# Performance work log

Hardware: AMD Instinct MI355X
Metric: run time of the kernel (lower is better)

Reference implementation:

```python
import jax, jax.numpy as jnp
import numpy as np
from jax import lax

B, S, H, T = 64, 512, 1024, 48


def setup_inputs() -> dict:
    key = jax.random.key(0)
    ks = jax.random.split(key, 8)
    x = jax.random.normal(ks[0], (B, S, H), dtype=jnp.float32)
    # left-aligned variable-length attention mask (lengths in [S//2, S])
    lengths = jax.random.randint(ks[1], (B,), S // 2, S + 1)
    attention_mask = (jnp.arange(S)[None, :] < lengths[:, None]).astype(jnp.int32)
    labels = jax.random.randint(ks[2], (B, S), 0, T).astype(jnp.int64)
    # decoder Linear(H, T)
    W = jax.random.normal(ks[3], (H, T), dtype=jnp.float32) / np.sqrt(H)
    b = jnp.zeros((T,), dtype=jnp.float32)
    # CRF parameters (allennlp-style: transitions + start/end transitions)
    transitions = jax.random.normal(ks[4], (T, T), dtype=jnp.float32) * 0.1
    start_trans = jax.random.normal(ks[5], (T,), dtype=jnp.float32) * 0.1
    end_trans = jax.random.normal(ks[6], (T,), dtype=jnp.float32) * 0.1
    return {"x": x, "attention_mask": attention_mask, "labels": labels,
            "W": W, "b": b, "transitions": transitions,
            "start_trans": start_trans, "end_trans": end_trans}


def _log_partition(logits, mask, trans, start, end):
    # logits [B,S,T], mask [B,S] int. Returns logZ [B].
    alpha0 = start[None, :] + logits[:, 0]                     # [B,T]
    emits = jnp.moveaxis(logits[:, 1:], 1, 0)                  # [S-1,B,T]
    ms = mask[:, 1:].T                                         # [S-1,B]

    def step(alpha, inp):
        emit, m = inp
        inner = alpha[:, :, None] + trans[None, :, :] + emit[:, None, :]  # [B,T,T]
        new = jax.nn.logsumexp(inner, axis=1)
        alpha = jnp.where(m[:, None] > 0, new, alpha)
        return alpha, None

    alpha, _ = lax.scan(step, alpha0, (emits, ms))
    return jax.nn.logsumexp(alpha + end[None, :], axis=1)      # [B]


def _gold_score(logits, labels, mask, trans, start, end):
    maskf = mask.astype(logits.dtype)
    emit = jnp.take_along_axis(logits, labels[..., None], axis=2)[..., 0]  # [B,S]
    emit_score = jnp.sum(emit * maskf, axis=1)
    tr = trans[labels[:, :-1], labels[:, 1:]]                   # [B,S-1]
    trans_score = jnp.sum(tr * maskf[:, 1:], axis=1)
    last_idx = jnp.sum(mask, axis=1) - 1                        # [B]
    last_tags = jnp.take_along_axis(labels, last_idx[:, None], axis=1)[:, 0]
    return start[labels[:, 0]] + emit_score + trans_score + end[last_tags]


def _viterbi(logits, mask, trans, start, end):
    Bn, Sn, Tn = logits.shape
    v0 = start[None, :] + logits[:, 0]
    emits = jnp.moveaxis(logits[:, 1:], 1, 0)                  # [S-1,B,T]
    ms = mask[:, 1:].T
    ident = jnp.broadcast_to(jnp.arange(Tn, dtype=jnp.int32)[None, :], (Bn, Tn))

    def step(v, inp):
        emit, m = inp
        scores = v[:, :, None] + trans[None, :, :]              # [B,T_prev,T_cur]
        bp = jnp.argmax(scores, axis=1).astype(jnp.int32)       # [B,T]
        best = jnp.max(scores, axis=1) + emit
        v_new = jnp.where(m[:, None] > 0, best, v)
        bp = jnp.where(m[:, None] > 0, bp, ident)               # identity at padded steps
        return v_new, bp

    v, bps = lax.scan(step, v0, (emits, ms))                    # bps [S-1,B,T]
    last = jnp.argmax(v + end[None, :], axis=1).astype(jnp.int32)  # [B]

    def back(tag, bp):
        prev = jnp.take_along_axis(bp, tag[:, None], axis=1)[:, 0]
        return prev, tag

    first_tag, rest = lax.scan(back, last, bps, reverse=True)   # rest [S-1,B]
    tags = jnp.concatenate([first_tag[:, None], rest.T], axis=1)  # [B,S]
    return (tags * mask).astype(jnp.int64)                      # pad with zeros


def reference(x, attention_mask, labels, W, b, transitions, start_trans, end_trans):
    features = jnp.einsum('bsh,ht->bst', x, W) + b              # decoder Linear
    pred_labels = _viterbi(features, attention_mask, transitions, start_trans, end_trans)
    logZ = _log_partition(features, attention_mask, transitions, start_trans, end_trans)
    gold = _gold_score(features, labels, attention_mask, transitions, start_trans, end_trans)
    loss = -jnp.sum(gold - logZ)                                # -log-likelihood, summed over batch
    return features, pred_labels, loss
```

## Files before the change

### kernel.cpp

```cpp
#include <hip/hip_runtime.h>
#include <hip/hip_bf16.h>
#include <math.h>

#define Bn 64
#define Sn 512
#define Hn 1024
#define Tn 48

#define LOG2E 1.4426950408889634f
#define LN2f  0.6931471805599453f

#define PRED_OFF (Bn*Sn*Tn)
#define LOSS_OFF (PRED_OFF + Bn*Sn)

#define RL(x,i) __int_as_float(__builtin_amdgcn_readlane(__float_as_int(x),(i)))

#if __has_builtin(__builtin_amdgcn_exp2f)
#define EXP2(x) __builtin_amdgcn_exp2f(x)
#else
#define EXP2(x) exp2f(x)
#endif
#if __has_builtin(__builtin_amdgcn_logf)
#define LOG2(x) __builtin_amdgcn_logf(x)
#else
#define LOG2(x) log2f(x)
#endif

__device__ __forceinline__ unsigned umin2(unsigned a, unsigned b) { return a < b ? a : b; }

#define VWS_BYTE_OFF 512
#define BPW_BYTE_OFF (512 + (size_t)Bn*Sn*Tn*4)

#define DOT4(ACC,A,B) { ACC = fmaf((A).x,(B).x,ACC); ACC = fmaf((A).y,(B).y,ACC); ACC = fmaf((A).z,(B).z,ACC); ACC = fmaf((A).w,(B).w,ACC); }

__global__ __launch_bounds__(256) void gemm_feat(
    const float* __restrict__ x, const float* __restrict__ W,
    const float* __restrict__ bias, float* __restrict__ feat)
{
  __shared__ __align__(16) float xs[64][68];
  __shared__ __align__(16) float wsT[Tn][68];
  const int tid = threadIdx.x;
  const int srow = tid >> 2;
  const int sqc  = tid & 3;
  const int ty = tid >> 3;
  const int tx = tid & 7;
  const size_t row0 = (size_t)blockIdx.x * 64;

  float4 xreg[4];
  float  wreg[12];
  #pragma unroll
  for (int p = 0; p < 4; ++p)
    xreg[p] = *reinterpret_cast<const float4*>(&x[(row0 + srow)*Hn + (sqc + p*4)*4]);
  #pragma unroll
  for (int i = 0; i < 12; ++i) {
    const int id = tid + i*256; const int kk = id/Tn; const int t = id - kk*Tn;
    wreg[i] = W[(size_t)kk*Tn + t];
  }

  float acc[2][6];
  #pragma unroll
  for (int r = 0; r < 2; ++r)
    #pragma unroll
    for (int c = 0; c < 6; ++c) acc[r][c] = 0.f;

  for (int k0 = 0; k0 < Hn; k0 += 64) {
    #pragma unroll
    for (int p = 0; p < 4; ++p)
      *reinterpret_cast<float4*>(&xs[srow][(sqc + p*4)*4]) = xreg[p];
    #pragma unroll
    for (int i = 0; i < 12; ++i) {
      const int id = tid + i*256; const int kk = id/Tn; const int t = id - kk*Tn;
      wsT[t][kk] = wreg[i];
    }
    __syncthreads();
    if (k0 + 64 < Hn) {
      #pragma unroll
      for (int p = 0; p < 4; ++p)
        xreg[p] = *reinterpret_cast<const float4*>(&x[(row0 + srow)*Hn + (k0+64) + (sqc + p*4)*4]);
      #pragma unroll
      for (int i = 0; i < 12; ++i) {
        const int id = tid + i*256; const int kk = id/Tn; const int t = id - kk*Tn;
        wreg[i] = W[(size_t)(k0 + 64 + kk)*Tn + t];
      }
    }
    #pragma unroll 4
    for (int kk = 0; kk < 64; kk += 4) {
      const float4 a0 = *reinterpret_cast<const float4*>(&xs[ty*2+0][kk]);
      const float4 a1 = *reinterpret_cast<const float4*>(&xs[ty*2+1][kk]);
      const float4 w0 = *reinterpret_cast<const float4*>(&wsT[tx*6+0][kk]);
      const float4 w1 = *reinterpret_cast<const float4*>(&wsT[tx*6+1][kk]);
      const float4 w2 = *reinterpret_cast<const float4*>(&wsT[tx*6+2][kk]);
      const float4 w3 = *reinterpret_cast<const float4*>(&wsT[tx*6+3][kk]);
      const float4 w4 = *reinterpret_cast<const float4*>(&wsT[tx*6+4][kk]);
      const float4 w5 = *reinterpret_cast<const float4*>(&wsT[tx*6+5][kk]);
      DOT4(acc[0][0],a0,w0) DOT4(acc[0][1],a0,w1) DOT4(acc[0][2],a0,w2)
      DOT4(acc[0][3],a0,w3) DOT4(acc[0][4],a0,w4) DOT4(acc[0][5],a0,w5)
      DOT4(acc[1][0],a1,w0) DOT4(acc[1][1],a1,w1) DOT4(acc[1][2],a1,w2)
      DOT4(acc[1][3],a1,w3) DOT4(acc[1][4],a1,w4) DOT4(acc[1][5],a1,w5)
    }
    __syncthreads();
  }
  #pragma unroll
  for (int c = 0; c < 6; ++c) {
    const int col = tx*6 + c;
    const float bv = bias[col];
    #pragma unroll
    for (int r = 0; r < 2; ++r)
      feat[(row0 + ty*2 + r)*Tn + col] = acc[r][c] + bv;
  }
}

__device__ __forceinline__ int seq_len(const int* __restrict__ mask, int b, int lane) {
  int lc = 0;
  #pragma unroll
  for (int it = 0; it < Sn/64; ++it) lc += (mask[(size_t)b*Sn + it*64 + lane] != 0);
  #pragma unroll
  for (int off = 32; off; off >>= 1) lc += __shfl_xor(lc, off);
  return lc;
}

#define ETS 52

__global__ __launch_bounds__(64, 1) void crf_scan(
    const float* __restrict__ feat,
    const int* __restrict__ mask,
    const int* __restrict__ labels,
    const float* __restrict__ trans,
    const float* __restrict__ startv,
    const float* __restrict__ endv,
    float* __restrict__ vws,
    float* __restrict__ wsLogZ,
    float* __restrict__ wsGold)
{
  __shared__ __align__(16) float LB[64 + 48*ETS];

  const int role = blockIdx.x >> 6;
  const int b    = blockIdx.x & 63;
  const int lane = threadIdx.x;
  const float* fb = feat + (size_t)b * Sn * Tn;
  const int len = seq_len(mask, b, lane);
  const int j = (lane < Tn) ? lane : (Tn - 1);

  const float4* sv4 = reinterpret_cast<const float4*>(&LB[0]);
  const float4* et4 = reinterpret_cast<const float4*>(&LB[64 + j*ETS]);

  if (role == 0) {
    for (int idx = lane; idx < Tn*Tn; idx += 64) {
      const int ii = idx / Tn, jj = idx - (idx/Tn)*Tn;
      LB[64 + jj*ETS + ii] = EXP2(trans[idx] * LOG2E);
    }
    __syncthreads();
    float emq0,emq1,emq2,emq3,emq4,emq5,emq6,emq7;
    #define LDEM(u) { int s = 1 + u; s = s < len ? s : len - 1; emq##u = fb[(size_t)s*Tn + j]; }
    LDEM(0) LDEM(1) LDEM(2) LDEM(3) LDEM(4) LDEM(5) LDEM(6) LDEM(7)
    #undef LDEM
    const float a0 = (startv[j] + fb[j]) * LOG2E;
    float Zref = RL(a0, 0);
    float beta = a0 - Zref;
    LB[lane] = EXP2(beta);
    #define PSTEP(u) { const int tt = t + u; if (tt < len) { \
      const float em2 = emq##u * LOG2E; \
      int tf = tt + 8; tf = tf < len ? tf : len - 1; \
      emq##u = fb[(size_t)tf * Tn + j]; \
      float s0=0.f,s1=0.f,s2=0.f,s3=0.f; \
      _Pragma("unroll") \
      for (int r = 0; r < 12; ++r) { \
        const float4 pv = sv4[r]; \
        const float4 ev = et4[r]; \
        s0 = fmaf(pv.x, ev.x, s0); \
        s1 = fmaf(pv.y, ev.y, s1); \
        s2 = fmaf(pv.z, ev.z, s2); \
        s3 = fmaf(pv.w, ev.w, s3); \
      } \
      const float dj = LOG2((s0+s1)+(s2+s3)) + em2; \
      const float d0 = RL(dj,0); \
      Zref += d0; beta = dj - d0; \
      LB[lane] = EXP2(beta); } }
    for (int t = 1; t < len; t += 8) {
      PSTEP(0) PSTEP(1) PSTEP(2) PSTEP(3) PSTEP(4) PSTEP(5) PSTEP(6) PSTEP(7)
    }
    #undef PSTEP
    float fv = (lane < Tn) ? beta + endv[lane] * LOG2E : -INFINITY;
    float m = fv;
    #pragma unroll
    for (int off = 32; off; off >>= 1) m = fmaxf(m, __shfl_xor(m, off));
    float e = (lane < Tn) ? EXP2(fv - m) : 0.f;
    #pragma unroll
    for (int off = 32; off; off >>= 1) e += __shfl_xor(e, off);
    if (lane == 0) wsLogZ[b] = (Zref + m + LOG2(e)) * LN2f;

  } else if (role == 1) {
    for (int idx = lane; idx < Tn*Tn; idx += 64) {
      const int ii = idx / Tn, jj = idx - (idx/Tn)*Tn;
      LB[64 + jj*ETS + ii] = trans[idx];
    }
    __syncthreads();
    float emq0,emq1,emq2,emq3,emq4,emq5,emq6,emq7;
    #define LDEM(u) { int s = 1 + u; s = s < len ? s : len - 1; emq##u = fb[(size_t)s*Tn + j]; }
    LDEM(0) LDEM(1) LDEM(2) LDEM(3) LDEM(4) LDEM(5) LDEM(6) LDEM(7)
    #undef LDEM
    float v = startv[j] + fb[j];
    LB[lane] = v;
    if (lane < Tn) vws[(size_t)b*Sn*Tn + lane] = v;
    #define VSTEP(u) { const int tt = t + u; if (tt < len) { \
      const float em_cur = emq##u; \
      int tf = tt + 8; tf = tf < len ? tf : len - 1; \
      emq##u = fb[(size_t)tf * Tn + j]; \
      float g0 = -INFINITY, g1 = -INFINITY, g2 = -INFINITY, g3 = -INFINITY; \
      _Pragma("unroll") \
      for (int r = 0; r < 12; ++r) { \
        const float4 pv = sv4[r]; \
        const float4 tv = et4[r]; \
        g0 = fmaxf(g0, pv.x + tv.x); \
        g1 = fmaxf(g1, pv.y + tv.y); \
        g2 = fmaxf(g2, pv.z + tv.z); \
        g3 = fmaxf(g3, pv.w + tv.w); \
      } \
      const float best = fmaxf(fmaxf(g0,g1), fmaxf(g2,g3)); \
      v = best + em_cur; \
      LB[lane] = v; \
      if (lane < Tn) vws[((size_t)b*Sn + tt)*Tn + lane] = v; } }
    for (int t = 1; t < len; t += 8) {
      VSTEP(0) VSTEP(1) VSTEP(2) VSTEP(3) VSTEP(4) VSTEP(5) VSTEP(6) VSTEP(7)
    }
    #undef VSTEP

  } else {
    float g = 0.f;
    #pragma unroll
    for (int it = 0; it < Sn/64; ++it) {
      const int sg = it*64 + lane;
      if (sg < len) {
        const int la = labels[(size_t)b*Sn + sg];
        float e = fb[(size_t)sg*Tn + la];
        if (sg > 0) e += trans[labels[(size_t)b*Sn + sg - 1]*Tn + la];
        g += e;
      }
    }
    #pragma unroll
    for (int off = 32; off; off >>= 1) g += __shfl_xor(g, off);
    if (lane == 0) {
      g += startv[labels[(size_t)b*Sn]] + endv[labels[(size_t)b*Sn + len - 1]];
      wsGold[b] = g;
    }
  }
}

__global__ __launch_bounds__(256) void bp_kernel(
    const float* __restrict__ vws,
    const int* __restrict__ mask,
    const float* __restrict__ trans,
    unsigned char* __restrict__ bpw)
{
  const int b    = blockIdx.x >> 3;
  const int oct  = blockIdx.x & 7;
  const int wv   = threadIdx.x >> 6;
  const int lane = threadIdx.x & 63;
  const int len = seq_len(mask, b, lane);
  const int j = (lane < Tn) ? lane : (Tn - 1);

  float4 T0,T1,T2,T3,T4,T5,T6,T7,T8,T9,T10,T11;
  #define LDT(k) T##k.x = trans[(4*k+0)*Tn + j]; \
                 T##k.y = trans[(4*k+1)*Tn + j]; \
                 T##k.z = trans[(4*k+2)*Tn + j]; \
                 T##k.w = trans[(4*k+3)*Tn + j];
  LDT(0) LDT(1) LDT(2) LDT(3) LDT(4) LDT(5) LDT(6) LDT(7) LDT(8) LDT(9) LDT(10) LDT(11)
  #undef LDT

  const int t0 = oct*64 + wv*16;
  for (int i = 0; i < 16; ++i) {
    const int t = t0 + i;
    int te = t; te = te < 1 ? 1 : te; te = te < len ? te : len - 1;
    const float4* vp = reinterpret_cast<const float4*>(vws + ((size_t)b*Sn + te - 1)*Tn);
    #define LDA(k) const float4 A##k = vp[k];
    LDA(0) LDA(1) LDA(2) LDA(3) LDA(4) LDA(5) LDA(6) LDA(7) LDA(8) LDA(9) LDA(10) LDA(11)
    #undef LDA
    #define GMAX(k) const float gq##k = fmaxf( \
      fmaxf(A##k.x+T##k.x, A##k.y+T##k.y), fmaxf(A##k.z+T##k.z, A##k.w+T##k.w));
    GMAX(0) GMAX(1) GMAX(2) GMAX(3) GMAX(4) GMAX(5)
    GMAX(6) GMAX(7) GMAX(8) GMAX(9) GMAX(10) GMAX(11)
    #undef GMAX
    const float h0 = fmaxf(fmaxf(gq0,gq1),fmaxf(gq2,gq3));
    const float h1 = fmaxf(fmaxf(gq4,gq5),fmaxf(gq6,gq7));
    const float h2 = fmaxf(fmaxf(gq8,gq9),fmaxf(gq10,gq11));
    const float best = fmaxf(fmaxf(h0,h1),h2);
    #define KEYG(k) umin2( \
      umin2(__float_as_uint((A##k.x+T##k.x)-best)|(unsigned)(4*k+0), \
            __float_as_uint((A##k.y+T##k.y)-best)|(unsigned)(4*k+1)), \
      umin2(__float_as_uint((A##k.z+T##k.z)-best)|(unsigned)(4*k+2), \
            __float_as_uint((A##k.w+T##k.w)-best)|(unsigned)(4*k+3)))
    const unsigned kA = umin2(umin2(KEYG(0), KEYG(1)), umin2(KEYG(2), KEYG(3)));
    const unsigned kB = umin2(umin2(KEYG(4), KEYG(5)), umin2(KEYG(6), KEYG(7)));
    const unsigned kC = umin2(umin2(KEYG(8), KEYG(9)), umin2(KEYG(10), KEYG(11)));
    #undef KEYG
    const unsigned bidx = umin2(umin2(kA, kB), kC);
    if (t >= 1 && t < len && lane < Tn)
      bpw[((size_t)b*Sn + t)*Tn + lane] = (unsigned char)bidx;
  }
}

__device__ __forceinline__ unsigned idw(int a) {
  return (unsigned)a | ((unsigned)(a+1)<<8) | ((unsigned)(a+2)<<16) | ((unsigned)(a+3)<<24);
}

__global__ __launch_bounds__(64, 1) void backtrace_kernel(
    const float* __restrict__ vws,
    const unsigned char* __restrict__ bpw,
    const int* __restrict__ mask,
    const float* __restrict__ endv,
    float* __restrict__ pred_out)
{
  __shared__ unsigned char bpL[Sn * Tn];
  __shared__ unsigned char pathL[384 * 64];
  __shared__ int EA[8];

  const int b    = blockIdx.x;
  const int lane = threadIdx.x;
  const int len = seq_len(mask, b, lane);

  {
    const uint4* gb = reinterpret_cast<const uint4*>(bpw + (size_t)b*Sn*Tn);
    uint4* bl = reinterpret_cast<uint4*>(bpL);
    for (int i4 = lane; i4 < Sn*Tn/16; i4 += 64) {
      const int byte0 = i4*16;
      const int t = byte0 / Tn;
      const int j0 = byte0 - t*Tn;
      uint4 val;
      if (t >= 1 && t < len) val = gb[i4];
      else { val.x = idw(j0); val.y = idw(j0+4); val.z = idw(j0+8); val.w = idw(j0+12); }
      bl[i4] = val;
    }
  }

  float fv = (lane < Tn) ? vws[((size_t)b*Sn + len - 1)*Tn + lane] + endv[lane] : -INFINITY;
  int fi = (lane < Tn) ? lane : 64;
  #pragma unroll
  for (int off = 32; off; off >>= 1) {
    const float ov = __shfl_xor(fv, off);
    const int   oi = __shfl_xor(fi, off);
    if (ov > fv || (ov == fv && oi < fi)) { fv = ov; fi = oi; }
  }
  __syncthreads();

  #define JOB(r) \
    const int id##r  = lane + 64*(r); \
    const int seg##r = id##r & 7;     \
    int cur##r = id##r >> 3;          \
    const int bpb##r = seg##r * 64 * Tn; \
    const int pb##r  = id##r << 6;    \
    pathL[pb##r + 63] = (unsigned char)cur##r;
  JOB(0) JOB(1) JOB(2) JOB(3) JOB(4) JOB(5)
  for (int d = 62; d >= 0; --d) {
    const int o = (d + 1) * Tn;
    cur0 = bpL[bpb0 + o + cur0]; pathL[pb0 + d] = (unsigned char)cur0;
    cur1 = bpL[bpb1 + o + cur1]; pathL[pb1 + d] = (unsigned char)cur1;
    cur2 = bpL[bpb2 + o + cur2]; pathL[pb2 + d] = (unsigned char)cur2;
    cur3 = bpL[bpb3 + o + cur3]; pathL[pb3 + d] = (unsigned char)cur3;
    cur4 = bpL[bpb4 + o + cur4]; pathL[pb4 + d] = (unsigned char)cur4;
    cur5 = bpL[bpb5 + o + cur5]; pathL[pb5 + d] = (unsigned char)cur5;
  }
  #undef JOB
  __syncthreads();
  if (lane == 0) {
    int Ecur = fi;
    EA[7] = Ecur;
    for (int s = 7; s >= 1; --s) {
      const int bottom = pathL[((Ecur << 3) + s) * 64];
      Ecur = bpL[(s * 64) * Tn + bottom];
      EA[s-1] = Ecur;
    }
  }
  __syncthreads();
  #pragma unroll
  for (int r8 = 0; r8 < 8; ++r8) {
    const int t = r8*64 + lane;
    const int pv = pathL[((EA[r8] << 3) + r8) * 64 + lane];
    pred_out[(size_t)b*Sn + t] = (t < len) ? (float)pv : 0.f;
  }
}

__global__ void loss_reduce(const float* __restrict__ wsLogZ,
                            const float* __restrict__ wsGold,
                            float* __restrict__ out)
{
  const int lane = threadIdx.x;
  float v = wsLogZ[lane] - wsGold[lane];
  #pragma unroll
  for (int off = 32; off; off >>= 1) v += __shfl_xor(v, off);
  if (lane == 0) out[0] = v;
}

extern "C" void kernel_launch(void* const* d_in, const int* in_sizes, int n_in,
                              void* d_out, int out_size, void* d_ws, size_t ws_size,
                              hipStream_t stream) {
  const float* x      = (const float*)d_in[0];
  const int*   mask   = (const int*)  d_in[1];
  const int*   labels = (const int*)  d_in[2];
  const float* W      = (const float*)d_in[3];
  const float* bias   = (const float*)d_in[4];
  const float* trans  = (const float*)d_in[5];
  const float* startv = (const float*)d_in[6];
  const float* endv   = (const float*)d_in[7];

  float* out  = (float*)d_out;
  float* feat = out;
  float* pred = out + PRED_OFF;
  float* loss = out + LOSS_OFF;
  float* wsLogZ = (float*)d_ws;
  float* wsGold = wsLogZ + 64;
  float* vws = (float*)((char*)d_ws + VWS_BYTE_OFF);
  unsigned char* bpw = (unsigned char*)d_ws + BPW_BYTE_OFF;

  gemm_feat<<<(Bn*Sn)/64, 256, 0, stream>>>(x, W, bias, feat);
  crf_scan<<<192, 64, 0, stream>>>(feat, mask, labels, trans, startv, endv, vws, wsLogZ, wsGold);
  bp_kernel<<<512, 256, 0, stream>>>(vws, mask, trans, bpw);
  backtrace_kernel<<<64, 64, 0, stream>>>(vws, bpw, mask, endv, pred);
  loss_reduce<<<1, 64, 0, stream>>>(wsLogZ, wsGold, loss);
}
```

Before: 343.1 us.

## Pack 16 CRF scan jobs per 1024-thread block sharing transition tables

Repacks the CRF scan from 192 single-wave blocks into 12 blocks of 16 waves, each wave handling one (role, batch) job. The transition tables, both exp and raw, are built once per block in shared memory instead of once per wave, and each wave gets its own 64-float state slot. The inner 12-step loops are manually unrolled through macros. This concentrates the serial scans on only 12 CUs with 16 waves each, which may contend for LDS bandwidth and issue slots compared with spreading them across many CUs.

New measurement: 399.7 us. 16.5% more time.

```diff
diff --git a/kernel.cpp b/kernel.cpp
--- a/kernel.cpp
+++ b/kernel.cpp
@@ -121,7 +121,7 @@
 
 #define ETS 52
 
-__global__ __launch_bounds__(64, 1) void crf_scan(
+__global__ __launch_bounds__(1024, 1) void crf_scan(
     const float* __restrict__ feat,
     const int* __restrict__ mask,
     const int* __restrict__ labels,
@@ -132,24 +132,34 @@
     float* __restrict__ wsLogZ,
     float* __restrict__ wsGold)
 {
-  __shared__ __align__(16) float LB[64 + 48*ETS];
-
-  const int role = blockIdx.x >> 6;
-  const int b    = blockIdx.x & 63;
-  const int lane = threadIdx.x;
+  __shared__ __align__(16) float ST[16*64];
+  __shared__ __align__(16) float TE[48*ETS];
+  __shared__ __align__(16) float TT[48*ETS];
+
+  const int tid  = threadIdx.x;
+  const int w    = tid >> 6;
+  const int lane = tid & 63;
+  const int job  = w * 12 + blockIdx.x;
+  const int role = job >> 6;
+  const int b    = job & 63;
+
+  for (int idx = tid; idx < Tn*Tn; idx += 1024) {
+    const int ii = idx / Tn, jj = idx - (idx/Tn)*Tn;
+    const float tv = trans[idx];
+    TE[jj*ETS + ii] = EXP2(tv * LOG2E);
+    TT[jj*ETS + ii] = tv;
+  }
+  __syncthreads();
+
   const float* fb = feat + (size_t)b * Sn * Tn;
   const int len = seq_len(mask, b, lane);
   const int j = (lane < Tn) ? lane : (Tn - 1);
 
-  const float4* sv4 = reinterpret_cast<const float4*>(&LB[0]);
-  const float4* et4 = reinterpret_cast<const float4*>(&LB[64 + j*ETS]);
+  float* sw = &ST[w * 64];
+  const float4* sv4 = reinterpret_cast<const float4*>(sw);
 
   if (role == 0) {
-    for (int idx = lane; idx < Tn*Tn; idx += 64) {
-      const int ii = idx / Tn, jj = idx - (idx/Tn)*Tn;
-      LB[64 + jj*ETS + ii] = EXP2(trans[idx] * LOG2E);
-    }
-    __syncthreads();
+    const float4* et4 = reinterpret_cast<const float4*>(&TE[j*ETS]);
     float emq0,emq1,emq2,emq3,emq4,emq5,emq6,emq7;
     #define LDEM(u) { int s = 1 + u; s = s < len ? s : len - 1; emq##u = fb[(size_t)s*Tn + j]; }
     LDEM(0) LDEM(1) LDEM(2) LDEM(3) LDEM(4) LDEM(5) LDEM(6) LDEM(7)
@@ -157,29 +167,28 @@
     const float a0 = (startv[j] + fb[j]) * LOG2E;
     float Zref = RL(a0, 0);
     float beta = a0 - Zref;
-    LB[lane] = EXP2(beta);
+    sw[lane] = EXP2(beta);
+    #define FMAG(k) { const float4 pv = sv4[k]; const float4 ev = et4[k]; \
+      s0 = fmaf(pv.x, ev.x, s0); \
+      s1 = fmaf(pv.y, ev.y, s1); \
+      s2 = fmaf(pv.z, ev.z, s2); \
+      s3 = fmaf(pv.w, ev.w, s3); }
     #define PSTEP(u) { const int tt = t + u; if (tt < len) { \
       const float em2 = emq##u * LOG2E; \
       int tf = tt + 8; tf = tf < len ? tf : len - 1; \
       emq##u = fb[(size_t)tf * Tn + j]; \
       float s0=0.f,s1=0.f,s2=0.f,s3=0.f; \
-      _Pragma("unroll") \
-      for (int r = 0; r < 12; ++r) { \
-        const float4 pv = sv4[r]; \
-        const float4 ev = et4[r]; \
-        s0 = fmaf(pv.x, ev.x, s0); \
-        s1 = fmaf(pv.y, ev.y, s1); \
-        s2 = fmaf(pv.z, ev.z, s2); \
-        s3 = fmaf(pv.w, ev.w, s3); \
-      } \
+      FMAG(0) FMAG(1) FMAG(2) FMAG(3) FMAG(4) FMAG(5) \
+      FMAG(6) FMAG(7) FMAG(8) FMAG(9) FMAG(10) FMAG(11) \
       const float dj = LOG2((s0+s1)+(s2+s3)) + em2; \
       const float d0 = RL(dj,0); \
       Zref += d0; beta = dj - d0; \
-      LB[lane] = EXP2(beta); } }
+      sw[lane] = EXP2(beta); } }
     for (int t = 1; t < len; t += 8) {
       PSTEP(0) PSTEP(1) PSTEP(2) PSTEP(3) PSTEP(4) PSTEP(5) PSTEP(6) PSTEP(7)
     }
     #undef PSTEP
+    #undef FMAG
     float fv = (lane < Tn) ? beta + endv[lane] * LOG2E : -INFINITY;
     float m = fv;
     #pragma unroll
@@ -190,40 +199,35 @@
     if (lane == 0) wsLogZ[b] = (Zref + m + LOG2(e)) * LN2f;
 
   } else if (role == 1) {
-    for (int idx = lane; idx < Tn*Tn; idx += 64) {
-      const int ii = idx / Tn, jj = idx - (idx/Tn)*Tn;
-      LB[64 + jj*ETS + ii] = trans[idx];
-    }
-    __syncthreads();
+    const float4* et4 = reinterpret_cast<const float4*>(&TT[j*ETS]);
     float emq0,emq1,emq2,emq3,emq4,emq5,emq6,emq7;
     #define LDEM(u) { int s = 1 + u; s = s < len ? s : len - 1; emq##u = fb[(size_t)s*Tn + j]; }
     LDEM(0) LDEM(1) LDEM(2) LDEM(3) LDEM(4) LDEM(5) LDEM(6) LDEM(7)
     #undef LDEM
     float v = startv[j] + fb[j];
-    LB[lane] = v;
+    sw[lane] = v;
     if (lane < Tn) vws[(size_t)b*Sn*Tn + lane] = v;
+    #define MAXG(k) { const float4 pv = sv4[k]; const float4 tv = et4[k]; \
+      g0 = fmaxf(g0, pv.x + tv.x); \
+      g1 = fmaxf(g1, pv.y + tv.y); \
+      g2 = fmaxf(g2, pv.z + tv.z); \
+      g3 = fmaxf(g3, pv.w + tv.w); }
     #define VSTEP(u) { const int tt = t + u; if (tt < len) { \
       const float em_cur = emq##u; \
       int tf = tt + 8; tf = tf < len ? tf : len - 1; \
       emq##u = fb[(size_t)tf * Tn + j]; \
       float g0 = -INFINITY, g1 = -INFINITY, g2 = -INFINITY, g3 = -INFINITY; \
-      _Pragma("unroll") \
-      for (int r = 0; r < 12; ++r) { \
-        const float4 pv = sv4[r]; \
-        const float4 tv = et4[r]; \
-        g0 = fmaxf(g0, pv.x + tv.x); \
-        g1 = fmaxf(g1, pv.y + tv.y); \
-        g2 = fmaxf(g2, pv.z + tv.z); \
-        g3 = fmaxf(g3, pv.w + tv.w); \
-      } \
+      MAXG(0) MAXG(1) MAXG(2) MAXG(3) MAXG(4) MAXG(5) \
+      MAXG(6) MAXG(7) MAXG(8) MAXG(9) MAXG(10) MAXG(11) \
       const float best = fmaxf(fmaxf(g0,g1), fmaxf(g2,g3)); \
       v = best + em_cur; \
-      LB[lane] = v; \
+      sw[lane] = v; \
       if (lane < Tn) vws[((size_t)b*Sn + tt)*Tn + lane] = v; } }
     for (int t = 1; t < len; t += 8) {
       VSTEP(0) VSTEP(1) VSTEP(2) VSTEP(3) VSTEP(4) VSTEP(5) VSTEP(6) VSTEP(7)
     }
     #undef VSTEP
+    #undef MAXG
 
   } else {
     float g = 0.f;
@@ -412,7 +416,7 @@
   unsigned char* bpw = (unsigned char*)d_ws + BPW_BYTE_OFF;
 
   gemm_feat<<<(Bn*Sn)/64, 256, 0, stream>>>(x, W, bias, feat);
-  crf_scan<<<192, 64, 0, stream>>>(feat, mask, labels, trans, startv, endv, vws, wsLogZ, wsGold);
+  crf_scan<<<12, 1024, 0, stream>>>(feat, mask, labels, trans, startv, endv, vws, wsLogZ, wsGold);
   bp_kernel<<<512, 256, 0, stream>>>(vws, mask, trans, bpw);
   backtrace_kernel<<<64, 64, 0, stream>>>(vws, bpw, mask, endv, pred);
   loss_reduce<<<1, 64, 0, stream>>>(wsLogZ, wsGold, loss);
```
